# Kernel tuning notes

Hardware: AMD Instinct MI355X
Metric: run time of the kernel (lower is better)

## Reference

```python
import jax, jax.numpy as jnp
import numpy as np
from jax import lax


def _b3_kernel_2d(dtype=jnp.float32):
    k1 = jnp.array([1.0 / 16.0, 1.0 / 4.0, 3.0 / 8.0, 1.0 / 4.0, 1.0 / 16.0], dtype=dtype)
    return jnp.outer(k1, k1)  # (5, 5)


def _dilated_b3_conv(x, kernel_2d, dilation):
    # PyTorch Conv2d(kernel_size=5, dilation=d, padding=2*d, padding_mode='reflect')
    pad = 2 * dilation
    xp = jnp.pad(x, ((0, 0), (0, 0), (pad, pad), (pad, pad)), mode='reflect')
    k = kernel_2d[None, None, :, :]  # (O=1, I=1, 5, 5)
    return lax.conv_general_dilated(
        xp, k,
        window_strides=(1, 1),
        padding='VALID',
        rhs_dilation=(dilation, dilation),
        dimension_numbers=('NCHW', 'OIHW', 'NCHW'),
    )


def setup_inputs() -> dict:
    key = jax.random.key(0)
    B, H, W = 16, 1024, 1024
    x = jax.random.normal(key, (B, 1, H, W), dtype=jnp.float32)
    kernel_2d = _b3_kernel_2d(jnp.float32)
    return {"x": x, "kernel_2d": kernel_2d, "n_scales": 5}


def reference(x, kernel_2d, n_scales):
    # a trous starlet transform: detail_j = c_j - c_{j+1}; last channel = coarse
    detail_scales = []
    coarse = x
    for scale_idx in range(n_scales - 1):
        dilation = 2 ** scale_idx
        next_coarse = _dilated_b3_conv(coarse, kernel_2d, dilation)
        detail_scales.append(coarse - next_coarse)
        coarse = next_coarse
    all_scales = detail_scales + [coarse]
    return jnp.concatenate(all_scales, axis=1)  # (B, n_scales, H, W)
```

## Files before the change

### kernel.cpp

```cpp
#include <hip/hip_runtime.h>

#define TX 64
#define TY 64

template<int D>
__global__ __launch_bounds__(256)
void starlet_scale(const float* __restrict__ in, long in_bs,
                   float* __restrict__ det,      long det_bs,
                   float* __restrict__ coa,      long coa_bs)
{
    constexpr int H = 1024, W = 1024;
    constexpr int R  = 2 * D;
    constexpr int LW = TX + 2 * R;
    constexpr int LH = TY + 2 * R;
    constexpr int LS = LW + 1;

    __shared__ float tile[LH * LS];
    __shared__ float htmp[LH * TX];

    const int tid = threadIdx.x;
    const int bx  = blockIdx.x * TX;
    const int by  = blockIdx.y * TY;
    const int b   = blockIdx.z;

    const float* __restrict__ inp = in + (long)b * in_bs;

    const float k0 = 0.0625f;
    const float k1 = 0.25f;
    const float k2 = 0.375f;

    for (int i = tid; i < LH * LW; i += 256) {
        int ly = i / LW;
        int lx = i - ly * LW;
        int gy = by - R + ly;
        gy = (gy < 0) ? -gy : ((gy >= H) ? (2 * H - 2 - gy) : gy);
        int gx = bx - R + lx;
        gx = (gx < 0) ? -gx : ((gx >= W) ? (2 * W - 2 - gx) : gx);
        tile[ly * LS + lx] = inp[(long)gy * W + gx];
    }
    __syncthreads();

    for (int i = tid; i < LH * TX; i += 256) {
        int r = i >> 6;
        int x = i & (TX - 1);
        const float* t = &tile[r * LS + x];
        htmp[i] = k0 * (t[0] + t[4 * D]) + k1 * (t[D] + t[3 * D]) + k2 * t[2 * D];
    }
    __syncthreads();

    for (int i = tid; i < TY * TX; i += 256) {
        int y = i >> 6;
        int x = i & (TX - 1);
        const float* h = &htmp[y * TX + x];
        float conv = k0 * (h[0] + h[4 * D * TX])
                   + k1 * (h[D * TX] + h[3 * D * TX])
                   + k2 * h[2 * D * TX];
        float center = tile[(y + R) * LS + (x + R)];
        long gidx = (long)(by + y) * W + (bx + x);
        det[(long)b * det_bs + gidx] = center - conv;
        coa[(long)b * coa_bs + gidx] = conv;
    }
}

extern "C" void kernel_launch(void* const* d_in, const int* in_sizes, int n_in,
                              void* d_out, int out_size, void* d_ws, size_t ws_size,
                              hipStream_t stream) {
    const float* x = (const float*)d_in[0];
    float* out = (float*)d_out;
    float* ws  = (float*)d_ws;

    const long HW = 1024L * 1024L;
    const long OB = 5 * HW;

    dim3 grid(1024 / TX, 1024 / TY, 16);
    dim3 block(256);

    starlet_scale<1><<<grid, block, 0, stream>>>(x, HW, out + 0 * HW, OB, ws, HW);
    starlet_scale<2><<<grid, block, 0, stream>>>(ws, HW, out + 1 * HW, OB, out + 4 * HW, OB);
    starlet_scale<4><<<grid, block, 0, stream>>>(out + 4 * HW, OB, out + 2 * HW, OB, ws, HW);
    starlet_scale<8><<<grid, block, 0, stream>>>(ws, HW, out + 3 * HW, OB, out + 4 * HW, OB);
}
```

Baseline: 513.2 us.

## Fuse all four starlet scales into one kernel with a 32-pixel halo tile

Replaces four separate per-scale launches with one kernel. Each block loads a 128x128 tile (a 64x64 output plus a 32-pixel reflected halo) into LDS once and runs all four dilated separable passes in place, with float4-vectorised LDS access. This removes the global-memory round trips of the intermediate coarse images and the workspace traffic. In exchange it recomputes a large halo region per tile, needs about 135KB of LDS per 1024-thread block (so occupancy is low), and relies on symmetric-kernel reflection staying consistent across scales at image borders.

```diff
diff --git a/kernel.cpp b/kernel.cpp
--- a/kernel.cpp
+++ b/kernel.cpp
@@ -1,65 +1,145 @@
 #include <hip/hip_runtime.h>
 
-#define TX 64
-#define TY 64
+
+constexpr int H  = 1024, W = 1024;
+constexpr int TS = 64;
+constexpr int HALO = 32;
+constexpr int RW = 128;
+constexpr int LSV = 33;
+constexpr int NT = 1024;
+
+static_assert(2 * RW * LSV * 16 <= 160 * 1024, "LDS budget");
+
+__device__ __forceinline__ int reflect_i(int g, int n) {
+    g = (g < 0) ? -g : g;
+    return (g >= n) ? (2 * n - 2 - g) : g;
+}
 
 template<int D>
-__global__ __launch_bounds__(256)
-void starlet_scale(const float* __restrict__ in, long in_bs,
-                   float* __restrict__ det,      long det_bs,
-                   float* __restrict__ coa,      long coa_bs)
+__device__ __forceinline__ void scale_pass(float4* __restrict__ A4, float4* __restrict__ B4,
+                                           int tid, int bx, int by,
+                                           float* __restrict__ det, float* __restrict__ coa)
 {
-    constexpr int H = 1024, W = 1024;
-    constexpr int R  = 2 * D;
-    constexpr int LW = TX + 2 * R;
-    constexpr int LH = TY + 2 * R;
-    constexpr int LS = LW + 1;
+    const float k0 = 0.0625f, k1 = 0.25f, k2 = 0.375f;
+    constexpr int Q  = 32 - 2 * D;
+    constexpr int HR = RW - 4 * D;
+    constexpr int HTASKS = HR * Q;
 
-    __shared__ float tile[LH * LS];
-    __shared__ float htmp[LH * TX];
-
-    const int tid = threadIdx.x;
-    const int bx  = blockIdx.x * TX;
-    const int by  = blockIdx.y * TY;
-    const int b   = blockIdx.z;
-
-    const float* __restrict__ inp = in + (long)b * in_bs;
-
-    const float k0 = 0.0625f;
-    const float k1 = 0.25f;
-    const float k2 = 0.375f;
-
-    for (int i = tid; i < LH * LW; i += 256) {
-        int ly = i / LW;
-        int lx = i - ly * LW;
-        int gy = by - R + ly;
-        gy = (gy < 0) ? -gy : ((gy >= H) ? (2 * H - 2 - gy) : gy);
-        int gx = bx - R + lx;
-        gx = (gx < 0) ? -gx : ((gx >= W) ? (2 * W - 2 - gx) : gx);
-        tile[ly * LS + lx] = inp[(long)gy * W + gx];
+    for (int t = tid; t < HTASKS; t += NT) {
+        int r    = 2 * D + t / Q;
+        int qx   = D + t % Q;
+        int base = r * LSV + qx;
+        float4 o;
+        if constexpr (D >= 4) {
+            float4 t0 = A4[base - D / 2];
+            float4 t1 = A4[base - D / 4];
+            float4 t2 = A4[base];
+            float4 t3 = A4[base + D / 4];
+            float4 t4 = A4[base + D / 2];
+            o.x = k0 * (t0.x + t4.x) + k1 * (t1.x + t3.x) + k2 * t2.x;
+            o.y = k0 * (t0.y + t4.y) + k1 * (t1.y + t3.y) + k2 * t2.y;
+            o.z = k0 * (t0.z + t4.z) + k1 * (t1.z + t3.z) + k2 * t2.z;
+            o.w = k0 * (t0.w + t4.w) + k1 * (t1.w + t3.w) + k2 * t2.w;
+        } else {
+            float4 v0 = A4[base - 1], v1 = A4[base], v2 = A4[base + 1];
+            float f[12] = {v0.x, v0.y, v0.z, v0.w,
+                           v1.x, v1.y, v1.z, v1.w,
+                           v2.x, v2.y, v2.z, v2.w};
+            float oo[4];
+            #pragma unroll
+            for (int i = 0; i < 4; ++i) {
+                if constexpr (D == 1)
+                    oo[i] = k0 * (f[i + 2] + f[i + 6]) + k1 * (f[i + 3] + f[i + 5]) + k2 * f[i + 4];
+                else
+                    oo[i] = k0 * (f[i]     + f[i + 8]) + k1 * (f[i + 2] + f[i + 6]) + k2 * f[i + 4];
+            }
+            o.x = oo[0]; o.y = oo[1]; o.z = oo[2]; o.w = oo[3];
+        }
+        B4[base] = o;
     }
     __syncthreads();
 
-    for (int i = tid; i < LH * TX; i += 256) {
-        int r = i >> 6;
-        int x = i & (TX - 1);
-        const float* t = &tile[r * LS + x];
-        htmp[i] = k0 * (t[0] + t[4 * D]) + k1 * (t[D] + t[3 * D]) + k2 * t[2 * D];
+    constexpr int NC = RW / D - 8;
+    constexpr int GR = NC / 4;
+    constexpr int VTASKS = D * GR * Q;
+    for (int t = tid; t < VTASKS; t += NT) {
+        int q  = t % Q;
+        int u  = t / Q;
+        int c  = u % D;
+        int g  = u / D;
+        int qx = D + q;
+        float4 rr[8];
+        #pragma unroll
+        for (int m = 0; m < 8; ++m) {
+            int r = 4 * D + c + (4 * g + m - 2) * D;
+            rr[m] = B4[r * LSV + qx];
+        }
+        #pragma unroll
+        for (int k = 0; k < 4; ++k) {
+            float4 acc;
+            acc.x = k0 * (rr[k].x + rr[k+4].x) + k1 * (rr[k+1].x + rr[k+3].x) + k2 * rr[k+2].x;
+            acc.y = k0 * (rr[k].y + rr[k+4].y) + k1 * (rr[k+1].y + rr[k+3].y) + k2 * rr[k+2].y;
+            acc.z = k0 * (rr[k].z + rr[k+4].z) + k1 * (rr[k+1].z + rr[k+3].z) + k2 * rr[k+2].z;
+            acc.w = k0 * (rr[k].w + rr[k+4].w) + k1 * (rr[k+1].w + rr[k+3].w) + k2 * rr[k+2].w;
+            int r  = 4 * D + c + (4 * g + k) * D;
+            int ai = r * LSV + qx;
+            int x  = 4 * qx;
+            bool center = (r >= HALO) && (r < HALO + TS) && (x >= HALO) && (x < HALO + TS);
+            if (center) {
+                float4 old = A4[ai];
+                float4 d = {old.x - acc.x, old.y - acc.y, old.z - acc.z, old.w - acc.w};
+                long gofs = (long)(by - HALO + r) * W + (bx - HALO + x);
+                *(float4*)(det + gofs) = d;
+                if constexpr (D == 8) *(float4*)(coa + gofs) = acc;
+            }
+            A4[ai] = acc;
+        }
+    }
+    __syncthreads();
+}
+
+__global__ __launch_bounds__(NT)
+void starlet_fused(const float* __restrict__ in, float* __restrict__ out)
+{
+    __shared__ float4 Abuf[RW * LSV];
+    __shared__ float4 Bbuf[RW * LSV];
+    float* A = (float*)Abuf;
+
+    const int tid = threadIdx.x;
+    const int bx  = blockIdx.x * TS;
+    const int by  = blockIdx.y * TS;
+    const int b   = blockIdx.z;
+    const float* __restrict__ inp  = in  + (long)b * H * W;
+    float* __restrict__       outp = out + (long)b * 5L * H * W;
+
+    const bool interior = (bx >= HALO) && (bx + TS + HALO <= W) &&
+                          (by >= HALO) && (by + TS + HALO <= H);
+    if (interior) {
+        const float* src = inp + (long)(by - HALO) * W + (bx - HALO);
+        #pragma unroll
+        for (int k = 0; k < 4; ++k) {
+            int idx = tid + k * NT;
+            int r   = idx >> 5;
+            int cq  = idx & 31;
+            Abuf[r * LSV + cq] = *(const float4*)(src + (long)r * W + 4 * cq);
+        }
+    } else {
+        #pragma unroll
+        for (int k = 0; k < 16; ++k) {
+            int idx = tid + k * NT;
+            int r   = idx >> 7;
+            int cc  = idx & 127;
+            int gy  = reflect_i(by - HALO + r, H);
+            int gx  = reflect_i(bx - HALO + cc, W);
+            A[r * (4 * LSV) + cc] = inp[(long)gy * W + gx];
+        }
     }
     __syncthreads();
 
-    for (int i = tid; i < TY * TX; i += 256) {
-        int y = i >> 6;
-        int x = i & (TX - 1);
-        const float* h = &htmp[y * TX + x];
-        float conv = k0 * (h[0] + h[4 * D * TX])
-                   + k1 * (h[D * TX] + h[3 * D * TX])
-                   + k2 * h[2 * D * TX];
-        float center = tile[(y + R) * LS + (x + R)];
-        long gidx = (long)(by + y) * W + (bx + x);
-        det[(long)b * det_bs + gidx] = center - conv;
-        coa[(long)b * coa_bs + gidx] = conv;
-    }
+    scale_pass<1>(Abuf, Bbuf, tid, bx, by, outp + 0L * H * W, nullptr);
+    scale_pass<2>(Abuf, Bbuf, tid, bx, by, outp + 1L * H * W, nullptr);
+    scale_pass<4>(Abuf, Bbuf, tid, bx, by, outp + 2L * H * W, nullptr);
+    scale_pass<8>(Abuf, Bbuf, tid, bx, by, outp + 3L * H * W, outp + 4L * H * W);
 }
 
 extern "C" void kernel_launch(void* const* d_in, const int* in_sizes, int n_in,
@@ -67,16 +147,9 @@
                               hipStream_t stream) {
     const float* x = (const float*)d_in[0];
     float* out = (float*)d_out;
-    float* ws  = (float*)d_ws;
+    (void)in_sizes; (void)n_in; (void)d_ws; (void)ws_size; (void)out_size;
 
-    const long HW = 1024L * 1024L;
-    const long OB = 5 * HW;
-
-    dim3 grid(1024 / TX, 1024 / TY, 16);
-    dim3 block(256);
-
-    starlet_scale<1><<<grid, block, 0, stream>>>(x, HW, out + 0 * HW, OB, ws, HW);
-    starlet_scale<2><<<grid, block, 0, stream>>>(ws, HW, out + 1 * HW, OB, out + 4 * HW, OB);
-    starlet_scale<4><<<grid, block, 0, stream>>>(out + 4 * HW, OB, out + 2 * HW, OB, ws, HW);
-    starlet_scale<8><<<grid, block, 0, stream>>>(ws, HW, out + 3 * HW, OB, out + 4 * HW, OB);
+    dim3 grid(W / TS, H / TS, 16);
+    dim3 block(NT);
+    starlet_fused<<<grid, block, 0, stream>>>(x, out);
 }
```

Result: faster. 478.5 us (-6.8%).

## Vectorize starlet scale kernel with float4 LDS tiles and register-blocked vertical pass

Applied to the files above, without the earlier changes.

Rewrites each scale kernel so that interior tiles load from global memory with float4 accesses, skipping the per-element reflect arithmetic, and only border tiles use the scalar reflected path. The horizontal pass now works on float4 groups in LDS. The vertical pass lets each thread hold 8 rows in registers and produce 4 outputs, each written as a float4 store. This is meant to cut global and LDS instruction counts and make memory traffic wider, at the cost of more registers and more complex indexing. Launch bounds also request 4 blocks per CU.

```diff
diff --git a/kernel.cpp b/kernel.cpp
--- a/kernel.cpp
+++ b/kernel.cpp
@@ -1,64 +1,129 @@
 #include <hip/hip_runtime.h>
 
-#define TX 64
-#define TY 64
+
+constexpr int H  = 1024, W = 1024;
+constexpr int TS = 64;
+constexpr int NT = 256;
+
+template<int D> struct Cfg {
+    static constexpr int RY   = 2 * D;
+    static constexpr int RXV  = (2 * D + 3) / 4;
+    static constexpr int RX   = 4 * RXV;
+    static constexpr int ROWS = TS + 2 * RY;
+    static constexpr int AV   = 16 + 2 * RXV;
+    static constexpr int AS   = AV + 1;
+    static constexpr int BS   = 17;
+    static constexpr int LOGD = (D == 1) ? 0 : (D == 2) ? 1 : (D == 4) ? 2 : 3;
+};
+
+__device__ __forceinline__ int reflect_i(int g, int n) {
+    g = (g < 0) ? -g : g;
+    return (g >= n) ? (2 * n - 2 - g) : g;
+}
 
 template<int D>
-__global__ __launch_bounds__(256)
+__global__ __launch_bounds__(256, 4)
 void starlet_scale(const float* __restrict__ in, long in_bs,
                    float* __restrict__ det,      long det_bs,
                    float* __restrict__ coa,      long coa_bs)
 {
-    constexpr int H = 1024, W = 1024;
-    constexpr int R  = 2 * D;
-    constexpr int LW = TX + 2 * R;
-    constexpr int LH = TY + 2 * R;
-    constexpr int LS = LW + 1;
+    using C = Cfg<D>;
+    __shared__ float4 A4[C::ROWS * C::AS];
+    __shared__ float4 B4[C::ROWS * C::BS];
 
-    __shared__ float tile[LH * LS];
-    __shared__ float htmp[LH * TX];
+    static_assert(sizeof(float4) * (C::ROWS * C::AS + C::ROWS * C::BS) <= 160 * 1024, "LDS");
 
     const int tid = threadIdx.x;
-    const int bx  = blockIdx.x * TX;
-    const int by  = blockIdx.y * TY;
+    const int bx  = blockIdx.x * TS;
+    const int by  = blockIdx.y * TS;
     const int b   = blockIdx.z;
-
     const float* __restrict__ inp = in + (long)b * in_bs;
 
-    const float k0 = 0.0625f;
-    const float k1 = 0.25f;
-    const float k2 = 0.375f;
+    const float k0 = 0.0625f, k1 = 0.25f, k2 = 0.375f;
 
-    for (int i = tid; i < LH * LW; i += 256) {
-        int ly = i / LW;
-        int lx = i - ly * LW;
-        int gy = by - R + ly;
-        gy = (gy < 0) ? -gy : ((gy >= H) ? (2 * H - 2 - gy) : gy);
-        int gx = bx - R + lx;
-        gx = (gx < 0) ? -gx : ((gx >= W) ? (2 * W - 2 - gx) : gx);
-        tile[ly * LS + lx] = inp[(long)gy * W + gx];
+    const bool interior = (bx >= C::RX) && (bx + TS + C::RX <= W) &&
+                          (by >= C::RY) && (by + TS + C::RY <= H);
+    if (interior) {
+        const float* src = inp + (long)(by - C::RY) * W + (bx - C::RX);
+        for (int i = tid; i < C::ROWS * C::AV; i += NT) {
+            int r = i / C::AV, c = i - r * C::AV;
+            A4[r * C::AS + c] = *(const float4*)(src + (long)r * W + 4 * c);
+        }
+    } else {
+        float* Af = (float*)A4;
+        for (int i = tid; i < C::ROWS * 4 * C::AV; i += NT) {
+            int r  = i / (4 * C::AV), c = i - r * (4 * C::AV);
+            int gy = reflect_i(by - C::RY + r, H);
+            int gx = reflect_i(bx - C::RX + c, W);
+            Af[r * (4 * C::AS) + c] = inp[(long)gy * W + gx];
+        }
     }
     __syncthreads();
 
-    for (int i = tid; i < LH * TX; i += 256) {
-        int r = i >> 6;
-        int x = i & (TX - 1);
-        const float* t = &tile[r * LS + x];
-        htmp[i] = k0 * (t[0] + t[4 * D]) + k1 * (t[D] + t[3 * D]) + k2 * t[2 * D];
+    for (int i = tid; i < C::ROWS * 16; i += NT) {
+        int r = i >> 4, q = i & 15;
+        int base = r * C::AS + C::RXV + q;
+        float4 o;
+        if constexpr (D >= 4) {
+            constexpr int s = D / 4;
+            float4 t0 = A4[base - 2 * s], t1 = A4[base - s], t2 = A4[base];
+            float4 t3 = A4[base + s],     t4 = A4[base + 2 * s];
+            o.x = k0 * (t0.x + t4.x) + k1 * (t1.x + t3.x) + k2 * t2.x;
+            o.y = k0 * (t0.y + t4.y) + k1 * (t1.y + t3.y) + k2 * t2.y;
+            o.z = k0 * (t0.z + t4.z) + k1 * (t1.z + t3.z) + k2 * t2.z;
+            o.w = k0 * (t0.w + t4.w) + k1 * (t1.w + t3.w) + k2 * t2.w;
+        } else {
+            float4 v0 = A4[base - 1], v1 = A4[base], v2 = A4[base + 1];
+            float f[12] = {v0.x, v0.y, v0.z, v0.w,
+                           v1.x, v1.y, v1.z, v1.w,
+                           v2.x, v2.y, v2.z, v2.w};
+            float oo[4];
+            #pragma unroll
+            for (int j = 0; j < 4; ++j) {
+                if constexpr (D == 1)
+                    oo[j] = k0 * (f[j + 2] + f[j + 6]) + k1 * (f[j + 3] + f[j + 5]) + k2 * f[j + 4];
+                else
+                    oo[j] = k0 * (f[j]     + f[j + 8]) + k1 * (f[j + 2] + f[j + 6]) + k2 * f[j + 4];
+            }
+            o.x = oo[0]; o.y = oo[1]; o.z = oo[2]; o.w = oo[3];
+        }
+        B4[r * C::BS + q] = o;
     }
     __syncthreads();
 
-    for (int i = tid; i < TY * TX; i += 256) {
-        int y = i >> 6;
-        int x = i & (TX - 1);
-        const float* h = &htmp[y * TX + x];
-        float conv = k0 * (h[0] + h[4 * D * TX])
-                   + k1 * (h[D * TX] + h[3 * D * TX])
-                   + k2 * h[2 * D * TX];
-        float center = tile[(y + R) * LS + (x + R)];
-        long gidx = (long)(by + y) * W + (bx + x);
-        det[(long)b * det_bs + gidx] = center - conv;
-        coa[(long)b * coa_bs + gidx] = conv;
+    {
+        const int q = tid & 15;
+        const int u = tid >> 4;
+        const int c = u & (D - 1);
+        const int g = u >> C::LOGD;
+        const int r0 = c + 4 * g * D;
+
+        float4 rr[8];
+        #pragma unroll
+        for (int m = 0; m < 8; ++m)
+            rr[m] = B4[(r0 + m * D) * C::BS + q];
+
+        float* detp = det + (long)b * det_bs;
+        float* coap = coa + (long)b * coa_bs;
+
+        #pragma unroll
+        for (int k = 0; k < 4; ++k) {
+            float4 acc;
+            acc.x = k0 * (rr[k].x + rr[k+4].x) + k1 * (rr[k+1].x + rr[k+3].x) + k2 * rr[k+2].x;
+            acc.y = k0 * (rr[k].y + rr[k+4].y) + k1 * (rr[k+1].y + rr[k+3].y) + k2 * rr[k+2].y;
+            acc.z = k0 * (rr[k].z + rr[k+4].z) + k1 * (rr[k+1].z + rr[k+3].z) + k2 * rr[k+2].z;
+            acc.w = k0 * (rr[k].w + rr[k+4].w) + k1 * (rr[k+1].w + rr[k+3].w) + k2 * rr[k+2].w;
+
+            const int y = c + (4 * g + k) * D;
+            float4 old = A4[(C::RY + y) * C::AS + C::RXV + q];
+            float4 d;
+            d.x = old.x - acc.x; d.y = old.y - acc.y;
+            d.z = old.z - acc.z; d.w = old.w - acc.w;
+
+            const long gofs = (long)(by + y) * W + (bx + 4 * q);
+            *(float4*)(detp + gofs) = d;
+            *(float4*)(coap + gofs) = acc;
+        }
     }
 }
 
@@ -68,12 +133,13 @@
     const float* x = (const float*)d_in[0];
     float* out = (float*)d_out;
     float* ws  = (float*)d_ws;
+    (void)in_sizes; (void)n_in; (void)ws_size; (void)out_size;
 
     const long HW = 1024L * 1024L;
     const long OB = 5 * HW;
 
-    dim3 grid(1024 / TX, 1024 / TY, 16);
-    dim3 block(256);
+    dim3 grid(W / TS, H / TS, 16);
+    dim3 block(NT);
 
     starlet_scale<1><<<grid, block, 0, stream>>>(x, HW, out + 0 * HW, OB, ws, HW);
     starlet_scale<2><<<grid, block, 0, stream>>>(ws, HW, out + 1 * HW, OB, out + 4 * HW, OB);
```

After: 511.6 us. About the same (-0.3%).
